# Kernel optimization log

Hardware: AMD Instinct MI355X
Metric: run time of the kernel (lower is better)

Reference implementation:

```python
import jax, jax.numpy as jnp
import numpy as np

MAX_P = 20
MAX_N = 50
FDIM = 256
SCALE = 0.08
STEPS = 3


def _grid_sample_border(feat_hwc, grid):
    # feat_hwc: [B,H,W,C]; grid: [B,Q,2] normalized xy in [-1,1]
    # Bilinear grid_sample, padding_mode='border', align_corners=False (matches torch).
    B, H, W, C = feat_hwc.shape

    def one(fm, g):  # fm [H,W,C], g [Q,2]
        ix = jnp.clip(((g[:, 0] + 1.0) * W - 1.0) * 0.5, 0.0, W - 1.0)
        iy = jnp.clip(((g[:, 1] + 1.0) * H - 1.0) * 0.5, 0.0, H - 1.0)
        x0f = jnp.floor(ix); y0f = jnp.floor(iy)
        wx = (ix - x0f)[:, None]; wy = (iy - y0f)[:, None]
        x0 = x0f.astype(jnp.int32); y0 = y0f.astype(jnp.int32)
        x1 = jnp.minimum(x0 + 1, W - 1); y1 = jnp.minimum(y0 + 1, H - 1)
        f00 = fm[y0, x0]; f01 = fm[y0, x1]  # [Q,C]
        f10 = fm[y1, x0]; f11 = fm[y1, x1]
        top = f00 * (1.0 - wx) + f01 * wx
        bot = f10 * (1.0 - wx) + f11 * wx
        return top * (1.0 - wy) + bot * wy

    return jax.vmap(one)(feat_hwc, grid)


def setup_inputs() -> dict:
    key = jax.random.key(0)
    ks = jax.random.split(key, 12)
    d = {
        'p2': jax.random.normal(ks[0], (4, 256, 256, 256), jnp.float32),
        'p4': jax.random.normal(ks[1], (4, 256, 64, 64), jnp.float32),
        'iw1': jax.random.normal(ks[2], (16384, 512), jnp.float32) * 0.01,
        'ib1': jnp.zeros((512,), jnp.float32),
        'iw2': jax.random.normal(ks[3], (512, 1024), jnp.float32) * 0.04,
        'ib2': jnp.zeros((1024,), jnp.float32),
        'iw3': jax.random.normal(ks[4], (1024, 2000), jnp.float32) * 0.03,
        'ib3': jnp.zeros((2000,), jnp.float32),
        'rw1': jax.random.normal(ks[5], (258, 256), jnp.float32) * 0.06,
        'rb1': jnp.zeros((256,), jnp.float32),
        'rw2': jax.random.normal(ks[6], (256, 128), jnp.float32) * 0.06,
        'rb2': jnp.zeros((128,), jnp.float32),
        'rw3': jax.random.normal(ks[7], (128, 2), jnp.float32) * 0.09,
        'rb3': jnp.zeros((2,), jnp.float32),
        'vw1': jax.random.normal(ks[8], (100, 128), jnp.float32) * 0.1,
        'vb1': jnp.zeros((128,), jnp.float32),
        'vw2': jax.random.normal(ks[9], (128, 1), jnp.float32) * 0.09,
        'vb2': jnp.zeros((1,), jnp.float32),
    }
    return d


def reference(p2, p4, iw1, ib1, iw2, ib2, iw3, ib3,
              rw1, rb1, rw2, rb2, rw3, rb3, vw1, vb1, vw2, vb2):
    B = p4.shape[0]
    # AdaptiveAvgPool2d(8) on 64x64 -> mean over 8x8 blocks
    pooled = p4.reshape(B, FDIM, 8, 8, 8, 8).mean(axis=(3, 5))  # [B,C,8,8]
    flat = pooled.reshape(B, -1)  # [B, C*64]
    h = jax.nn.relu(flat @ iw1 + ib1)
    h = jax.nn.relu(h @ iw2 + ib2)
    init_polygons = jax.nn.sigmoid(h @ iw3 + ib3).reshape(B, MAX_P, MAX_N, 2)

    feat_hwc = jnp.transpose(p2, (0, 2, 3, 1))  # [B,H,W,C]
    polygons = init_polygons
    for _ in range(STEPS):
        coords = polygons.reshape(B, -1, 2)           # [B,Q,2] in [0,1]
        grid = coords * 2.0 - 1.0
        sampled = _grid_sample_border(feat_hwc, grid)  # [B,Q,C]
        inp = jnp.concatenate([sampled, coords], axis=-1)  # [B,Q,C+2]
        r = jax.nn.relu(inp @ rw1 + rb1)
        r = jax.nn.relu(r @ rw2 + rb2)
        disp = jnp.tanh(r @ rw3 + rb3).reshape(B, MAX_P, MAX_N, 2)
        bad = ~jnp.all(jnp.isfinite(disp))
        disp = jnp.where(bad, 0.0,
                         jnp.clip(disp * SCALE, -2.0 * SCALE, 2.0 * SCALE))
        polygons = jnp.clip(polygons + disp, 0.0, 1.0)

    poly_flat = polygons.reshape(B * MAX_P, MAX_N * 2)
    v = jax.nn.relu(poly_flat @ vw1 + vb1)
    validity = jax.nn.sigmoid(v @ vw2 + vb2).reshape(B, MAX_P)
    return polygons, validity, init_polygons
```

## Files before the change

### kernel.cpp

```cpp
#include <hip/hip_runtime.h>
#include <math.h>

#define WS_FLAT 0
#define WS_PART 65536
#define WS_H1   (65536 + 524288)
#define WS_H2   (WS_H1 + 2048)
#define WS_POLY (WS_H2 + 4096)

__global__ void pool_k(const float* __restrict__ p4, float* __restrict__ flat) {
    int o = blockIdx.x * blockDim.x + threadIdx.x;
    int b = o >> 14;
    int c = (o >> 6) & 255;
    int ij = o & 63;
    int i = ij >> 3, j = ij & 7;
    const float* base = p4 + (((size_t)(b * 256 + c) * 64 + i * 8) * 64 + j * 8);
    float s = 0.f;
    #pragma unroll
    for (int u = 0; u < 8; ++u) {
        const float4* r = (const float4*)(base + u * 64);
        float4 a = r[0], bb = r[1];
        s += a.x + a.y + a.z + a.w + bb.x + bb.y + bb.z + bb.w;
    }
    flat[o] = s * (1.0f / 64.0f);
}

__global__ void g1a_k(const float* __restrict__ flat, const float* __restrict__ iw1,
                      float* __restrict__ part) {
    __shared__ float sf[4][64];
    int tid = threadIdx.x;
    int kbase = blockIdx.x * 64;
    if (tid < 256) sf[tid >> 6][tid & 63] = flat[(tid >> 6) * 16384 + kbase + (tid & 63)];
    __syncthreads();
    float a0 = 0.f, a1 = 0.f, a2 = 0.f, a3 = 0.f;
    for (int k = 0; k < 64; ++k) {
        float w = iw1[(size_t)(kbase + k) * 512 + tid];
        a0 = fmaf(sf[0][k], w, a0);
        a1 = fmaf(sf[1][k], w, a1);
        a2 = fmaf(sf[2][k], w, a2);
        a3 = fmaf(sf[3][k], w, a3);
    }
    float* pp = part + (size_t)blockIdx.x * 2048;
    pp[tid] = a0; pp[512 + tid] = a1; pp[1024 + tid] = a2; pp[1536 + tid] = a3;
}

__global__ void g1b_k(const float* __restrict__ part, const float* __restrict__ ib1,
                      float* __restrict__ h1) {
    __shared__ float red[8][32];
    int tid = threadIdx.x;
    int cc = tid >> 5, oo = tid & 31;
    int o = blockIdx.x * 32 + oo;
    float s = 0.f;
    for (int i = 0; i < 32; ++i)
        s += part[(size_t)(cc + 8 * i) * 2048 + o];
    red[cc][oo] = s;
    __syncthreads();
    if (cc == 0) {
        float t = 0.f;
        #pragma unroll
        for (int c2 = 0; c2 < 8; ++c2) t += red[c2][oo];
        t += ib1[o & 511];
        h1[o] = fmaxf(t, 0.f);
    }
}

__global__ void g2_k(const float* __restrict__ h1, const float* __restrict__ iw2,
                     const float* __restrict__ ib2, float* __restrict__ h2) {
    __shared__ float sh[512];
    int tid = threadIdx.x;
    int b = blockIdx.x >> 2, jt = blockIdx.x & 3;
    sh[tid] = h1[b * 512 + tid];
    sh[tid + 256] = h1[b * 512 + 256 + tid];
    __syncthreads();
    int j = jt * 256 + tid;
    float acc = ib2[j];
    for (int k = 0; k < 512; ++k)
        acc = fmaf(sh[k], iw2[(size_t)k * 1024 + j], acc);
    h2[b * 1024 + j] = fmaxf(acc, 0.f);
}

__global__ void g3_k(const float* __restrict__ h2, const float* __restrict__ iw3,
                     const float* __restrict__ ib3, float* __restrict__ out_init,
                     float* __restrict__ poly) {
    int o = blockIdx.x * 256 + threadIdx.x;
    if (o >= 8000) return;
    int b = o / 2000, j = o % 2000;
    const float* h = h2 + b * 1024;
    float acc = ib3[j];
    for (int k = 0; k < 1024; ++k)
        acc = fmaf(h[k], iw3[(size_t)k * 2000 + j], acc);
    float s = 1.f / (1.f + expf(-acc));
    out_init[o] = s;
    poly[o] = s;
}

__global__ void __launch_bounds__(256) step_k(
    const float* __restrict__ p2,
    const float* __restrict__ rw1, const float* __restrict__ rb1,
    const float* __restrict__ rw2, const float* __restrict__ rb2,
    const float* __restrict__ rw3, const float* __restrict__ rb3,
    float* __restrict__ poly) {
    __shared__ __align__(16) float s_inp[258 * 8];
    __shared__ __align__(16) float s_r1[256 * 8];
    __shared__ __align__(16) float s_r2[128 * 8];
    int tid = threadIdx.x;
    int pt0 = blockIdx.x * 8;

    float val[8];
    #pragma unroll
    for (int pp = 0; pp < 8; ++pp) {
        int pt = pt0 + pp;
        int b = pt / 1000;
        float cx = poly[pt * 2], cy = poly[pt * 2 + 1];
        float ix = fminf(fmaxf(cx * 256.f - 0.5f, 0.f), 255.f);
        float iy = fminf(fmaxf(cy * 256.f - 0.5f, 0.f), 255.f);
        float x0f = floorf(ix), y0f = floorf(iy);
        int x0 = (int)x0f, y0 = (int)y0f;
        int x1 = min(x0 + 1, 255), y1 = min(y0 + 1, 255);
        float wx = ix - x0f, wy = iy - y0f;
        const float* fb = p2 + ((size_t)(b * 256 + tid) << 16);
        float f00 = fb[(y0 << 8) + x0], f01 = fb[(y0 << 8) + x1];
        float f10 = fb[(y1 << 8) + x0], f11 = fb[(y1 << 8) + x1];
        float top = f00 * (1.f - wx) + f01 * wx;
        float bot = f10 * (1.f - wx) + f11 * wx;
        val[pp] = top * (1.f - wy) + bot * wy;
    }
    ((float4*)&s_inp[tid * 8])[0] = make_float4(val[0], val[1], val[2], val[3]);
    ((float4*)&s_inp[tid * 8])[1] = make_float4(val[4], val[5], val[6], val[7]);
    if (tid < 16) {
        int p = tid >> 1, d = tid & 1;
        s_inp[(256 + d) * 8 + p] = poly[(pt0 + p) * 2 + d];
    }
    __syncthreads();

    {
        float bias = rb1[tid];
        float a0 = bias, a1 = bias, a2 = bias, a3 = bias;
        float a4 = bias, a5 = bias, a6 = bias, a7 = bias;
        for (int k = 0; k < 258; ++k) {
            float w = rw1[k * 256 + tid];
            float4 v0 = ((const float4*)&s_inp[k * 8])[0];
            float4 v1 = ((const float4*)&s_inp[k * 8])[1];
            a0 = fmaf(v0.x, w, a0); a1 = fmaf(v0.y, w, a1);
            a2 = fmaf(v0.z, w, a2); a3 = fmaf(v0.w, w, a3);
            a4 = fmaf(v1.x, w, a4); a5 = fmaf(v1.y, w, a5);
            a6 = fmaf(v1.z, w, a6); a7 = fmaf(v1.w, w, a7);
        }
        ((float4*)&s_r1[tid * 8])[0] =
            make_float4(fmaxf(a0, 0.f), fmaxf(a1, 0.f), fmaxf(a2, 0.f), fmaxf(a3, 0.f));
        ((float4*)&s_r1[tid * 8])[1] =
            make_float4(fmaxf(a4, 0.f), fmaxf(a5, 0.f), fmaxf(a6, 0.f), fmaxf(a7, 0.f));
    }
    __syncthreads();

    {
        int j = tid & 127, ph = tid >> 7;
        float bias = rb2[j];
        float c0 = bias, c1 = bias, c2 = bias, c3 = bias;
        for (int k = 0; k < 256; ++k) {
            float w = rw2[k * 128 + j];
            float4 v = ((const float4*)&s_r1[k * 8])[ph];
            c0 = fmaf(v.x, w, c0); c1 = fmaf(v.y, w, c1);
            c2 = fmaf(v.z, w, c2); c3 = fmaf(v.w, w, c3);
        }
        ((float4*)&s_r2[j * 8])[ph] =
            make_float4(fmaxf(c0, 0.f), fmaxf(c1, 0.f), fmaxf(c2, 0.f), fmaxf(c3, 0.f));
    }
    __syncthreads();

    if (tid < 16) {
        int p = tid >> 1, d = tid & 1;
        float acc = rb3[d];
        for (int k = 0; k < 128; ++k)
            acc = fmaf(s_r2[k * 8 + p], rw3[k * 2 + d], acc);
        float disp = tanhf(acc) * 0.08f;
        disp = fminf(fmaxf(disp, -0.16f), 0.16f);
        int idx = (pt0 + p) * 2 + d;
        float nv = poly[idx] + disp;
        poly[idx] = fminf(fmaxf(nv, 0.f), 1.f);
    }
}

__global__ void valid_k(const float* __restrict__ poly,
                        const float* __restrict__ vw1, const float* __restrict__ vb1,
                        const float* __restrict__ vw2, const float* __restrict__ vb2,
                        float* __restrict__ out) {
    __shared__ float sp[100];
    __shared__ float sred[2];
    int tid = threadIdx.x;
    int row = blockIdx.x;
    if (tid < 100) {
        float v = poly[row * 100 + tid];
        sp[tid] = v;
        out[row * 100 + tid] = v;
    }
    __syncthreads();
    float acc = vb1[tid];
    for (int k = 0; k < 100; ++k)
        acc = fmaf(sp[k], vw1[k * 128 + tid], acc);
    float pr = fmaxf(acc, 0.f) * vw2[tid];
    #pragma unroll
    for (int off = 32; off > 0; off >>= 1)
        pr += __shfl_down(pr, off, 64);
    if ((tid & 63) == 0) sred[tid >> 6] = pr;
    __syncthreads();
    if (tid == 0) {
        float s = sred[0] + sred[1] + vb2[0];
        out[8000 + row] = 1.f / (1.f + expf(-s));
    }
}

extern "C" void kernel_launch(void* const* d_in, const int* in_sizes, int n_in,
                              void* d_out, int out_size, void* d_ws, size_t ws_size,
                              hipStream_t stream) {
    const float* p2  = (const float*)d_in[0];
    const float* p4  = (const float*)d_in[1];
    const float* iw1 = (const float*)d_in[2];
    const float* ib1 = (const float*)d_in[3];
    const float* iw2 = (const float*)d_in[4];
    const float* ib2 = (const float*)d_in[5];
    const float* iw3 = (const float*)d_in[6];
    const float* ib3 = (const float*)d_in[7];
    const float* rw1 = (const float*)d_in[8];
    const float* rb1 = (const float*)d_in[9];
    const float* rw2 = (const float*)d_in[10];
    const float* rb2 = (const float*)d_in[11];
    const float* rw3 = (const float*)d_in[12];
    const float* rb3 = (const float*)d_in[13];
    const float* vw1 = (const float*)d_in[14];
    const float* vb1 = (const float*)d_in[15];
    const float* vw2 = (const float*)d_in[16];
    const float* vb2 = (const float*)d_in[17];
    float* out = (float*)d_out;
    float* ws = (float*)d_ws;
    float* flat = ws + WS_FLAT;
    float* part = ws + WS_PART;
    float* h1   = ws + WS_H1;
    float* h2   = ws + WS_H2;
    float* poly = ws + WS_POLY;

    pool_k<<<256, 256, 0, stream>>>(p4, flat);
    g1a_k<<<256, 512, 0, stream>>>(flat, iw1, part);
    g1b_k<<<64, 256, 0, stream>>>(part, ib1, h1);
    g2_k<<<16, 256, 0, stream>>>(h1, iw2, ib2, h2);
    g3_k<<<32, 256, 0, stream>>>(h2, iw3, ib3, out + 8080, poly);
    for (int s = 0; s < 3; ++s)
        step_k<<<500, 256, 0, stream>>>(p2, rw1, rb1, rw2, rb2, rw3, rb3, poly);
    valid_k<<<80, 128, 0, stream>>>(poly, vw1, vb1, vw2, vb2, out);
}
```

Measured before the change: 644.6 us.

## Transpose p2 to channel-last for coalesced sampling and split-K the MLP GEMVs

Adds a tiled shared-memory transpose that converts p2 from NCHW to NHWC in workspace on every call. The refinement step kernels then gather bilinear corners with contiguous per-channel reads instead of reads spaced 64K floats apart. The g2 and g3 GEMV kernels are split over K into four chunks with a shared-memory reduction, which launches 4x more blocks. The trade is a full 256MB read plus 256MB write of p2 on each call, and a much larger workspace requirement.

```diff
diff --git a/kernel.cpp b/kernel.cpp
--- a/kernel.cpp
+++ b/kernel.cpp
@@ -6,6 +6,38 @@
 #define WS_H1   (65536 + 524288)
 #define WS_H2   (WS_H1 + 2048)
 #define WS_POLY (WS_H2 + 4096)
+#define WS_P2T  1048576
+
+__global__ void __launch_bounds__(256) transpose_k(const float* __restrict__ in,
+                                                   float* __restrict__ out) {
+    __shared__ float t[64][65];
+    int tile = blockIdx.x;
+    int b  = tile >> 12;
+    int ct = (tile >> 10) & 3;
+    int xt = tile & 1023;
+    int c0 = ct << 6, yx0 = xt << 6;
+    int tid = threadIdx.x;
+
+    int jv = (tid & 15) << 2;
+    int i0 = tid >> 4;
+    const float* ip = in + (((size_t)(b * 256 + c0)) << 16) + yx0;
+    #pragma unroll
+    for (int ii = i0; ii < 64; ii += 16) {
+        float4 v = *(const float4*)(ip + ((size_t)ii << 16) + jv);
+        t[jv + 0][ii] = v.x; t[jv + 1][ii] = v.y;
+        t[jv + 2][ii] = v.z; t[jv + 3][ii] = v.w;
+    }
+    __syncthreads();
+
+    int iv = (tid & 15) << 2;
+    int j0 = tid >> 4;
+    float* op = out + ((size_t)b << 24) + ((size_t)yx0 << 8) + c0;
+    #pragma unroll
+    for (int jj = j0; jj < 64; jj += 16) {
+        float4 v = make_float4(t[jj][iv], t[jj][iv + 1], t[jj][iv + 2], t[jj][iv + 3]);
+        *(float4*)(op + ((size_t)jj << 8) + iv) = v;
+    }
+}
 
 __global__ void pool_k(const float* __restrict__ p4, float* __restrict__ flat) {
     int o = blockIdx.x * blockDim.x + threadIdx.x;
@@ -66,35 +98,56 @@
 __global__ void g2_k(const float* __restrict__ h1, const float* __restrict__ iw2,
                      const float* __restrict__ ib2, float* __restrict__ h2) {
     __shared__ float sh[512];
-    int tid = threadIdx.x;
-    int b = blockIdx.x >> 2, jt = blockIdx.x & 3;
+    __shared__ float red[4][64];
+    int tid = threadIdx.x;
+    int b = blockIdx.x >> 4, jt = blockIdx.x & 15;
     sh[tid] = h1[b * 512 + tid];
     sh[tid + 256] = h1[b * 512 + 256 + tid];
     __syncthreads();
-    int j = jt * 256 + tid;
-    float acc = ib2[j];
-    for (int k = 0; k < 512; ++k)
+    int j = (jt << 6) + (tid & 63);
+    int kc = tid >> 6;
+    float acc = 0.f;
+    for (int k = kc * 128; k < kc * 128 + 128; ++k)
         acc = fmaf(sh[k], iw2[(size_t)k * 1024 + j], acc);
-    h2[b * 1024 + j] = fmaxf(acc, 0.f);
+    red[kc][tid & 63] = acc;
+    __syncthreads();
+    if (kc == 0) {
+        float t = red[0][tid] + red[1][tid] + red[2][tid] + red[3][tid] + ib2[j];
+        h2[b * 1024 + j] = fmaxf(t, 0.f);
+    }
 }
 
 __global__ void g3_k(const float* __restrict__ h2, const float* __restrict__ iw3,
                      const float* __restrict__ ib3, float* __restrict__ out_init,
                      float* __restrict__ poly) {
-    int o = blockIdx.x * 256 + threadIdx.x;
-    if (o >= 8000) return;
-    int b = o / 2000, j = o % 2000;
+    __shared__ float sh[1024];
+    __shared__ float red[4][64];
+    int tid = threadIdx.x;
+    int b = blockIdx.x >> 5, jt = blockIdx.x & 31;
     const float* h = h2 + b * 1024;
-    float acc = ib3[j];
-    for (int k = 0; k < 1024; ++k)
-        acc = fmaf(h[k], iw3[(size_t)k * 2000 + j], acc);
-    float s = 1.f / (1.f + expf(-acc));
-    out_init[o] = s;
-    poly[o] = s;
+    sh[tid] = h[tid]; sh[tid + 256] = h[tid + 256];
+    sh[tid + 512] = h[tid + 512]; sh[tid + 768] = h[tid + 768];
+    __syncthreads();
+    int j = (jt << 6) + (tid & 63);
+    int kc = tid >> 6;
+    float acc = 0.f;
+    if (j < 2000) {
+        for (int k = kc * 256; k < kc * 256 + 256; ++k)
+            acc = fmaf(sh[k], iw3[(size_t)k * 2000 + j], acc);
+    }
+    red[kc][tid & 63] = acc;
+    __syncthreads();
+    if (kc == 0 && j < 2000) {
+        float t = red[0][tid] + red[1][tid] + red[2][tid] + red[3][tid] + ib3[j];
+        float s = 1.f / (1.f + expf(-t));
+        int o = b * 2000 + j;
+        out_init[o] = s;
+        poly[o] = s;
+    }
 }
 
 __global__ void __launch_bounds__(256) step_k(
-    const float* __restrict__ p2,
+    const float* __restrict__ p2t,
     const float* __restrict__ rw1, const float* __restrict__ rb1,
     const float* __restrict__ rw2, const float* __restrict__ rb2,
     const float* __restrict__ rw3, const float* __restrict__ rb3,
@@ -104,12 +157,13 @@
     __shared__ __align__(16) float s_r2[128 * 8];
     int tid = threadIdx.x;
     int pt0 = blockIdx.x * 8;
+    int b = pt0 / 1000;
+    const float* bt = p2t + ((size_t)b << 24);
 
     float val[8];
     #pragma unroll
     for (int pp = 0; pp < 8; ++pp) {
         int pt = pt0 + pp;
-        int b = pt / 1000;
         float cx = poly[pt * 2], cy = poly[pt * 2 + 1];
         float ix = fminf(fmaxf(cx * 256.f - 0.5f, 0.f), 255.f);
         float iy = fminf(fmaxf(cy * 256.f - 0.5f, 0.f), 255.f);
@@ -117,9 +171,11 @@
         int x0 = (int)x0f, y0 = (int)y0f;
         int x1 = min(x0 + 1, 255), y1 = min(y0 + 1, 255);
         float wx = ix - x0f, wy = iy - y0f;
-        const float* fb = p2 + ((size_t)(b * 256 + tid) << 16);
-        float f00 = fb[(y0 << 8) + x0], f01 = fb[(y0 << 8) + x1];
-        float f10 = fb[(y1 << 8) + x0], f11 = fb[(y1 << 8) + x1];
+        int r0 = (y0 << 16) + (x0 << 8);
+        int r1i = (y1 << 16) + (x0 << 8);
+        int dx = (x1 - x0) << 8;
+        float f00 = bt[r0 + tid],  f01 = bt[r0 + dx + tid];
+        float f10 = bt[r1i + tid], f11 = bt[r1i + dx + tid];
         float top = f00 * (1.f - wx) + f01 * wx;
         float bot = f10 * (1.f - wx) + f11 * wx;
         val[pp] = top * (1.f - wy) + bot * wy;
@@ -237,13 +293,15 @@
     float* h1   = ws + WS_H1;
     float* h2   = ws + WS_H2;
     float* poly = ws + WS_POLY;
+    float* p2t  = ws + WS_P2T;
 
     pool_k<<<256, 256, 0, stream>>>(p4, flat);
     g1a_k<<<256, 512, 0, stream>>>(flat, iw1, part);
     g1b_k<<<64, 256, 0, stream>>>(part, ib1, h1);
-    g2_k<<<16, 256, 0, stream>>>(h1, iw2, ib2, h2);
-    g3_k<<<32, 256, 0, stream>>>(h2, iw3, ib3, out + 8080, poly);
+    g2_k<<<64, 256, 0, stream>>>(h1, iw2, ib2, h2);
+    g3_k<<<128, 256, 0, stream>>>(h2, iw3, ib3, out + 8080, poly);
+    transpose_k<<<16384, 256, 0, stream>>>(p2, p2t);
     for (int s = 0; s < 3; ++s)
-        step_k<<<500, 256, 0, stream>>>(p2, rw1, rb1, rw2, rb2, rw3, rb3, poly);
+        step_k<<<500, 256, 0, stream>>>(p2t, rw1, rb1, rw2, rb2, rw3, rb3, poly);
     valid_k<<<80, 128, 0, stream>>>(poly, vw1, vb1, vw2, vb2, out);
 }
```

Measured after the change: 603.9 us. -6.3%, faster.
